# Performance work log

Hardware: AMD Instinct MI355X
Metric: run time of the kernel (lower is better)

The kernel has to match this reference:

```python
import jax, jax.numpy as jnp
import numpy as np

DIS_Z = 0.5     # depth search half-window (init kwarg dis_z)
NSAMPLE = 64    # max neighbors per query (init kwarg nsample)
B, N, M = 8, 16384, 2048


def setup_inputs() -> dict:
    key = jax.random.key(0)
    k1, k2 = jax.random.split(key)
    xyz1 = jax.random.normal(k1, (B, 3, N), dtype=jnp.float32)  # input points
    xyz2 = jax.random.normal(k2, (B, 3, M), dtype=jnp.float32)  # query points
    return {"xyz1": xyz1, "xyz2": xyz2}


def reference(xyz1, xyz2):
    """Depth-constrained radius search (semantics of query_depth_point CUDA kernel).

    For each query point q, scan input points j in order; if |z_j - z_q| < dis_z,
    record j. The first match pre-fills all nsample slots (ball-query convention),
    then subsequent matches overwrite slots 1..nsample-1. Stops after nsample
    matches. Returns idx (B,M,nsample) int64 and pts_cnt (B,M) int32.
    """
    n = xyz1.shape[2]
    z1 = xyz1[:, 2, :]                    # [B, N] input-point depths
    z2 = xyz2[:, 2, :]                    # [B, M] query-point depths
    # [B, M, N] depth-window mask (only the z coordinate is compared)
    mask = jnp.abs(z2[:, :, None] - z1[:, None, :]) < DIS_Z
    # Score earlier indices higher so top_k returns the FIRST nsample matches
    # in scan order; non-matches score 0.
    score = jnp.where(mask, n - jnp.arange(n, dtype=jnp.int32), 0)  # [B, M, N]
    vals, _ = jax.lax.top_k(score, NSAMPLE)   # [B, M, nsample], descending
    valid = vals > 0                          # slot k has a real (k-th) match
    idx_raw = n - vals                        # recover original index where valid
    first = idx_raw[..., 0:1]                 # index of first match (if any)
    cnt_total = jnp.sum(mask, axis=-1)        # [B, M] total matches
    pts_cnt = jnp.minimum(cnt_total, NSAMPLE).astype(jnp.int32)
    # Unfilled slots hold the first match index; if no match at all, stay 0.
    idx = jnp.where(valid, idx_raw,
                    jnp.where(cnt_total[..., None] > 0, first, 0)).astype(jnp.int64)
    return idx, pts_cnt
```

## Files before the change

### kernel.cpp

```cpp
#include <hip/hip_runtime.h>


#define QDP_B 8
#define QDP_N 16384
#define QDP_M 2048
#define QDP_NS 64
#define QDP_DISZ 0.5f
#define QDP_QPW 16

__device__ __forceinline__ void qdp_group(
    int cg, float zq, const float4& A, const float4& B,
    int lane, unsigned long long below,
    int& cnt, int& firstv, int* __restrict__ idx_out)
{
    const bool m0 = fabsf(A.x - zq) < QDP_DISZ;
    const bool m1 = fabsf(A.y - zq) < QDP_DISZ;
    const bool m2 = fabsf(A.z - zq) < QDP_DISZ;
    const bool m3 = fabsf(A.w - zq) < QDP_DISZ;
    const bool m4 = fabsf(B.x - zq) < QDP_DISZ;
    const bool m5 = fabsf(B.y - zq) < QDP_DISZ;
    const bool m6 = fabsf(B.z - zq) < QDP_DISZ;
    const bool m7 = fabsf(B.w - zq) < QDP_DISZ;

    const unsigned long long b0 = __ballot(m0);
    const unsigned long long b1 = __ballot(m1);
    const unsigned long long b2 = __ballot(m2);
    const unsigned long long b3 = __ballot(m3);
    const unsigned long long b4 = __ballot(m4);
    const unsigned long long b5 = __ballot(m5);
    const unsigned long long b6 = __ballot(m6);
    const unsigned long long b7 = __ballot(m7);
    const unsigned long long any = b0|b1|b2|b3|b4|b5|b6|b7;
    if (!any) return;

    const int mbyte = (int)m0 | ((int)m1<<1) | ((int)m2<<2) | ((int)m3<<3)
                    | ((int)m4<<4) | ((int)m5<<5) | ((int)m6<<6) | ((int)m7<<7);
    if (cnt == 0) {
        const int l0  = (int)__builtin_ctzll(any);
        const int mb0 = __shfl(mbyte, l0);
        firstv = cg + 8 * l0 + (int)__builtin_ctz((unsigned)mb0);
    }
    int r = cnt + __popcll(b0 & below) + __popcll(b1 & below)
                + __popcll(b2 & below) + __popcll(b3 & below)
                + __popcll(b4 & below) + __popcll(b5 & below)
                + __popcll(b6 & below) + __popcll(b7 & below);
    const int base = cg + 8 * lane;
    if (m0) { if (r < QDP_NS) idx_out[r] = base + 0; r++; }
    if (m1) { if (r < QDP_NS) idx_out[r] = base + 1; r++; }
    if (m2) { if (r < QDP_NS) idx_out[r] = base + 2; r++; }
    if (m3) { if (r < QDP_NS) idx_out[r] = base + 3; r++; }
    if (m4) { if (r < QDP_NS) idx_out[r] = base + 4; r++; }
    if (m5) { if (r < QDP_NS) idx_out[r] = base + 5; r++; }
    if (m6) { if (r < QDP_NS) idx_out[r] = base + 6; r++; }
    if (m7) { if (r < QDP_NS) idx_out[r] = base + 7; r++; }
    cnt += __popcll(b0) + __popcll(b1) + __popcll(b2) + __popcll(b3)
         + __popcll(b4) + __popcll(b5) + __popcll(b6) + __popcll(b7);
}

__global__ __launch_bounds__(256) void QueryDepthPoint_kernel(
    const float* __restrict__ xyz1,
    const float* __restrict__ xyz2,
    int* __restrict__ out_idx,
    int* __restrict__ out_cnt)
{
    const int lane = threadIdx.x & 63;
    const int wv   = (blockIdx.x << 2) + (threadIdx.x >> 6);
    const unsigned long long below = (1ull << lane) - 1ull;

    const int qbase = wv * QDP_QPW;
    const int b = qbase >> 11;
    const float* __restrict__ z1 = xyz1 + b * 3 * QDP_N + 2 * QDP_N;
    const float* __restrict__ z2 = xyz2 + b * 3 * QDP_M + 2 * QDP_M;

    const float zqv = z2[(qbase & (QDP_M - 1)) + (lane & (QDP_QPW - 1))];

    #pragma unroll 1
    for (int k = 0; k < QDP_QPW; ++k) {
        const float zq = __shfl(zqv, k);
        int* __restrict__ idx_out = out_idx + (size_t)(qbase + k) * QDP_NS;
        int cnt = 0, firstv = 0;

        #pragma unroll 1
        for (int c = 0; c < QDP_N; c += 2048) {
            const float* p = z1 + c + 8 * lane;
            const float4 a0 = ((const float4*)p)[0];
            const float4 b0 = ((const float4*)p)[1];
            const float4 a1 = ((const float4*)(p + 512))[0];
            const float4 b1 = ((const float4*)(p + 512))[1];
            const float4 a2 = ((const float4*)(p + 1024))[0];
            const float4 b2 = ((const float4*)(p + 1024))[1];
            const float4 a3 = ((const float4*)(p + 1536))[0];
            const float4 b3 = ((const float4*)(p + 1536))[1];

            qdp_group(c +    0, zq, a0, b0, lane, below, cnt, firstv, idx_out);
            if (cnt >= QDP_NS) break;
            qdp_group(c +  512, zq, a1, b1, lane, below, cnt, firstv, idx_out);
            if (cnt >= QDP_NS) break;
            qdp_group(c + 1024, zq, a2, b2, lane, below, cnt, firstv, idx_out);
            if (cnt >= QDP_NS) break;
            qdp_group(c + 1536, zq, a3, b3, lane, below, cnt, firstv, idx_out);
            if (cnt >= QDP_NS) break;
        }
        if (cnt > QDP_NS) cnt = QDP_NS;

        if (lane >= cnt) idx_out[lane] = firstv;
        if (lane == 0)   out_cnt[qbase + k] = cnt;
    }
}

extern "C" void kernel_launch(void* const* d_in, const int* in_sizes, int n_in,
                              void* d_out, int out_size, void* d_ws, size_t ws_size,
                              hipStream_t stream) {
    const float* xyz1 = (const float*)d_in[0];
    const float* xyz2 = (const float*)d_in[1];
    int* out = (int*)d_out;

    int* out_idx = out;
    int* out_cnt = out + (size_t)QDP_B * QDP_M * QDP_NS;

    QueryDepthPoint_kernel<<<256, 256, 0, stream>>>(xyz1, xyz2, out_idx, out_cnt);
}
```

Measured before the change: 85.70 us.

## Assign one query per wavefront and software-prefetch next chunk of depths

Instead of each wavefront serially processing 16 queries, the kernel now launches one wavefront per query (4096 blocks instead of 256), giving far more parallelism and wave-level latency hiding. The inner loop scans 1024 points per iteration and double-buffers the next chunk's loads in registers before processing the current one. The trade-off is more redundant reads of the z1 array across waves (mostly absorbed by cache) and some wasted prefetches past the early-exit point.

```diff
diff --git a/kernel.cpp b/kernel.cpp
--- a/kernel.cpp
+++ b/kernel.cpp
@@ -6,10 +6,9 @@
 #define QDP_M 2048
 #define QDP_NS 64
 #define QDP_DISZ 0.5f
-#define QDP_QPW 16
 
 __device__ __forceinline__ void qdp_group(
-    int cg, float zq, const float4& A, const float4& B,
+    int g, float zq, const float4& A, const float4& B,
     int lane, unsigned long long below,
     int& cnt, int& firstv, int* __restrict__ idx_out)
 {
@@ -38,13 +37,13 @@
     if (cnt == 0) {
         const int l0  = (int)__builtin_ctzll(any);
         const int mb0 = __shfl(mbyte, l0);
-        firstv = cg + 8 * l0 + (int)__builtin_ctz((unsigned)mb0);
+        firstv = g + 8 * l0 + (int)__builtin_ctz((unsigned)mb0);
     }
     int r = cnt + __popcll(b0 & below) + __popcll(b1 & below)
                 + __popcll(b2 & below) + __popcll(b3 & below)
                 + __popcll(b4 & below) + __popcll(b5 & below)
                 + __popcll(b6 & below) + __popcll(b7 & below);
-    const int base = cg + 8 * lane;
+    const int base = g + 8 * lane;
     if (m0) { if (r < QDP_NS) idx_out[r] = base + 0; r++; }
     if (m1) { if (r < QDP_NS) idx_out[r] = base + 1; r++; }
     if (m2) { if (r < QDP_NS) idx_out[r] = base + 2; r++; }
@@ -64,48 +63,43 @@
     int* __restrict__ out_cnt)
 {
     const int lane = threadIdx.x & 63;
-    const int wv   = (blockIdx.x << 2) + (threadIdx.x >> 6);
+    const int wid  = (blockIdx.x << 2) + (threadIdx.x >> 6);
+
+    const int b = wid >> 11;
+    const int q = wid & (QDP_M - 1);
+
+    const float zq = xyz2[b * 3 * QDP_M + 2 * QDP_M + q];
+    const float* __restrict__ z1 = xyz1 + b * 3 * QDP_N + 2 * QDP_N;
+    int* __restrict__ idx_out = out_idx + (size_t)wid * QDP_NS;
+
+    int cnt = 0, firstv = 0;
     const unsigned long long below = (1ull << lane) - 1ull;
+    const int lo = 8 * lane;
 
-    const int qbase = wv * QDP_QPW;
-    const int b = qbase >> 11;
-    const float* __restrict__ z1 = xyz1 + b * 3 * QDP_N + 2 * QDP_N;
-    const float* __restrict__ z2 = xyz2 + b * 3 * QDP_M + 2 * QDP_M;
-
-    const float zqv = z2[(qbase & (QDP_M - 1)) + (lane & (QDP_QPW - 1))];
+    float4 cA0 = ((const float4*)(z1 + lo))[0];
+    float4 cB0 = ((const float4*)(z1 + lo))[1];
+    float4 cA1 = ((const float4*)(z1 + 512 + lo))[0];
+    float4 cB1 = ((const float4*)(z1 + 512 + lo))[1];
 
     #pragma unroll 1
-    for (int k = 0; k < QDP_QPW; ++k) {
-        const float zq = __shfl(zqv, k);
-        int* __restrict__ idx_out = out_idx + (size_t)(qbase + k) * QDP_NS;
-        int cnt = 0, firstv = 0;
+    for (int c = 0; c < QDP_N; c += 1024) {
+        const int pn = (c + 1024) & (QDP_N - 1);
+        float4 nA0 = ((const float4*)(z1 + pn + lo))[0];
+        float4 nB0 = ((const float4*)(z1 + pn + lo))[1];
+        float4 nA1 = ((const float4*)(z1 + pn + 512 + lo))[0];
+        float4 nB1 = ((const float4*)(z1 + pn + 512 + lo))[1];
 
-        #pragma unroll 1
-        for (int c = 0; c < QDP_N; c += 2048) {
-            const float* p = z1 + c + 8 * lane;
-            const float4 a0 = ((const float4*)p)[0];
-            const float4 b0 = ((const float4*)p)[1];
-            const float4 a1 = ((const float4*)(p + 512))[0];
-            const float4 b1 = ((const float4*)(p + 512))[1];
-            const float4 a2 = ((const float4*)(p + 1024))[0];
-            const float4 b2 = ((const float4*)(p + 1024))[1];
-            const float4 a3 = ((const float4*)(p + 1536))[0];
-            const float4 b3 = ((const float4*)(p + 1536))[1];
+        qdp_group(c,       zq, cA0, cB0, lane, below, cnt, firstv, idx_out);
+        if (cnt >= QDP_NS) break;
+        qdp_group(c + 512, zq, cA1, cB1, lane, below, cnt, firstv, idx_out);
+        if (cnt >= QDP_NS) break;
 
-            qdp_group(c +    0, zq, a0, b0, lane, below, cnt, firstv, idx_out);
-            if (cnt >= QDP_NS) break;
-            qdp_group(c +  512, zq, a1, b1, lane, below, cnt, firstv, idx_out);
-            if (cnt >= QDP_NS) break;
-            qdp_group(c + 1024, zq, a2, b2, lane, below, cnt, firstv, idx_out);
-            if (cnt >= QDP_NS) break;
-            qdp_group(c + 1536, zq, a3, b3, lane, below, cnt, firstv, idx_out);
-            if (cnt >= QDP_NS) break;
-        }
-        if (cnt > QDP_NS) cnt = QDP_NS;
+        cA0 = nA0; cB0 = nB0; cA1 = nA1; cB1 = nB1;
+    }
+    if (cnt > QDP_NS) cnt = QDP_NS;
 
-        if (lane >= cnt) idx_out[lane] = firstv;
-        if (lane == 0)   out_cnt[qbase + k] = cnt;
-    }
+    if (lane >= cnt) idx_out[lane] = firstv;
+    if (lane == 0)   out_cnt[wid] = cnt;
 }
 
 extern "C" void kernel_launch(void* const* d_in, const int* in_sizes, int n_in,
@@ -118,5 +112,8 @@
     int* out_idx = out;
     int* out_cnt = out + (size_t)QDP_B * QDP_M * QDP_NS;
 
-    QueryDepthPoint_kernel<<<256, 256, 0, stream>>>(xyz1, xyz2, out_idx, out_cnt);
+    const int total_waves = QDP_B * QDP_M;
+    const int grid = total_waves / 4;
+
+    QueryDepthPoint_kernel<<<grid, 256, 0, stream>>>(xyz1, xyz2, out_idx, out_cnt);
 }
```

After: 72.32 us. -15.6%, faster.
